# Optimization experiments

Hardware: AMD Instinct MI355X
Metric: run time of the kernel (lower is better)

Reference implementation:

```python
import jax, jax.numpy as jnp
import numpy as np

Z_DIM = 64
K = 2048
N = 32768


def setup_inputs() -> dict:
    key = jax.random.key(0)
    k1, k2 = jax.random.split(key)
    x = jax.random.normal(k1, (N, Z_DIM), dtype=jnp.float32)
    # init.normal_(locs, std=sqrt(z_dim))
    locs = jax.random.normal(k2, (K, Z_DIM), dtype=jnp.float32) * np.sqrt(Z_DIM)
    logits = jnp.zeros((K,), dtype=jnp.float32)  # maxent buffer
    return {"x": x, "locs": locs, "logits": logits}


def reference(x, locs, logits):
    d = x.shape[-1]
    var = jnp.float32(d)  # scale = sqrt(z_dim) -> variance = z_dim
    # squared distances [N, K] via cdist expansion (avoids [N,K,d] intermediate)
    sq = (
        jnp.sum(x * x, axis=-1, keepdims=True)
        + jnp.sum(locs * locs, axis=-1)[None, :]
        - 2.0 * (x @ locs.T)
    )
    # Independent Normal log prob summed over z_dim
    log_norm_const = d * (0.5 * jnp.log(2.0 * jnp.pi) + 0.5 * jnp.log(var))
    comp_log_prob = -0.5 * sq / var - log_norm_const  # [N, K]
    mix_logits = jax.nn.log_softmax(logits)  # Categorical normalizes logits
    wlp = comp_log_prob + mix_logits  # weighted_log_prob, [N, K]
    log_prob = jax.nn.logsumexp(wlp, axis=-1)  # [N]
    modes = jnp.argmax(wlp, axis=-1)  # assign_modes, [N]
    quantized = locs[modes]  # hard_quantize, [N, z_dim]
    return log_prob, quantized
```

## Files before the change

### kernel.cpp

```cpp
#include <hip/hip_runtime.h>
#include <math.h>

#define N_SAMP 32768
#define K_COMP 2048
#define ZD 64
#define LNC 191.896324792608546f
#define LN2F 0.69314718055994531f
#define INV_LN2 1.44269504088896340f
#define S2C 0.02254211001388974f

#define KG 4
#define TILES (K_COMP / 16 / KG)

typedef __attribute__((ext_vector_type(8))) short short8;
typedef __attribute__((ext_vector_type(4))) float v4f;

#if __has_builtin(__builtin_amdgcn_exp2f)
#define EXP2(x) __builtin_amdgcn_exp2f(x)
#else
#define EXP2(x) exp2f(x)
#endif

__device__ inline unsigned short f2bf(float f) {
    unsigned int u = __float_as_uint(f);
    u += 0x7fffu + ((u >> 16) & 1u);
    return (unsigned short)(u >> 16);
}
__device__ inline float bf2f(unsigned short h) {
    return __uint_as_float(((unsigned int)h) << 16);
}

__global__ __launch_bounds__(256) void prep_kernel(
    const float* __restrict__ locs, const float* __restrict__ logits,
    float* __restrict__ ck2, float* __restrict__ lse_out,
    char* __restrict__ lf) {
    if (blockIdx.x < 32) {
        int gid = blockIdx.x * 256 + threadIdx.x;
        int T = gid >> 6;
        int l = gid & 63;
        int n = l & 15, q = l >> 4;
        int k = T * 16 + n;

        const float* src = locs + (size_t)k * ZD + q * 8;
        float4 u0 = *(const float4*)(src);
        float4 u1 = *(const float4*)(src + 4);
        float4 u2 = *(const float4*)(src + 32);
        float4 u3 = *(const float4*)(src + 36);
        float a[8] = {u0.x, u0.y, u0.z, u0.w, u1.x, u1.y, u1.z, u1.w};
        float b[8] = {u2.x, u2.y, u2.z, u2.w, u3.x, u3.y, u3.z, u3.w};

        short8 h0, h1, l0, l1;
        float sq = 0.f;
#pragma unroll
        for (int j = 0; j < 8; ++j) {
            unsigned short ha = f2bf(a[j]);
            h0[j] = (short)ha; l0[j] = (short)f2bf(a[j] - bf2f(ha));
            unsigned short hb = f2bf(b[j]);
            h1[j] = (short)hb; l1[j] = (short)f2bf(b[j] - bf2f(hb));
            sq = fmaf(a[j], a[j], sq);
            sq = fmaf(b[j], b[j], sq);
        }
        char* dst = lf + (size_t)T * 4096 + l * 16;
        *(short8*)(dst)        = h0;
        *(short8*)(dst + 1024) = h1;
        *(short8*)(dst + 2048) = l0;
        *(short8*)(dst + 3072) = l1;

        sq += __shfl_xor(sq, 16);
        sq += __shfl_xor(sq, 32);
        if (q == 0) ck2[k] = (logits[k] - sq * (1.0f / 128.0f)) * INV_LN2;
    } else {
        __shared__ float red[4];
        int tid = threadIdx.x;
        int wv = tid >> 6, ln = tid & 63;
        float lm = -INFINITY;
        for (int i = tid; i < K_COMP; i += 256) lm = fmaxf(lm, logits[i]);
#pragma unroll
        for (int d = 1; d < 64; d <<= 1) lm = fmaxf(lm, __shfl_xor(lm, d));
        if (ln == 0) red[wv] = lm;
        __syncthreads();
        float M = fmaxf(fmaxf(red[0], red[1]), fmaxf(red[2], red[3]));
        float ls = 0.f;
        for (int i = tid; i < K_COMP; i += 256) ls += __expf(logits[i] - M);
#pragma unroll
        for (int d = 1; d < 64; d <<= 1) ls += __shfl_xor(ls, d);
        __syncthreads();
        if (ln == 0) red[wv] = ls;
        __syncthreads();
        if (tid == 0) *lse_out = M + __logf(red[0] + red[1] + red[2] + red[3]);
    }
}

__global__ __launch_bounds__(256, 2) void mix_kernel(
    const float* __restrict__ x, const float* __restrict__ locs,
    const char* __restrict__ lf, const float* __restrict__ ck2,
    const float* __restrict__ lse_ptr, float* __restrict__ out) {

    __shared__ float sm[KG][64];
    __shared__ float ss[KG][64];
    __shared__ int   sa[KG][64];
    __shared__ int   amax_sh[64];

    const int tid  = threadIdx.x;
    const int lane = tid & 63;
    const int kg   = __builtin_amdgcn_readfirstlane(tid >> 6);
    const int n    = lane & 15;
    const int quad = lane >> 4;
    const int sbase = blockIdx.x * 64;

    short8 bh[4][2], bl[4][2];
    float xs[4];
#pragma unroll
    for (int bt = 0; bt < 4; ++bt) {
        const float* xp = x + (size_t)(sbase + bt * 16 + n) * ZD + quad * 8;
        float4 u0 = *(const float4*)(xp);
        float4 u1 = *(const float4*)(xp + 4);
        float4 u2 = *(const float4*)(xp + 32);
        float4 u3 = *(const float4*)(xp + 36);
        float a[8] = {u0.x, u0.y, u0.z, u0.w, u1.x, u1.y, u1.z, u1.w};
        float b[8] = {u2.x, u2.y, u2.z, u2.w, u3.x, u3.y, u3.z, u3.w};
        float p = 0.f;
#pragma unroll
        for (int j = 0; j < 8; ++j) {
            unsigned short h;
            h = f2bf(a[j]); bh[bt][0][j] = (short)h; bl[bt][0][j] = (short)f2bf(a[j] - bf2f(h));
            h = f2bf(b[j]); bh[bt][1][j] = (short)h; bl[bt][1][j] = (short)f2bf(b[j] - bf2f(h));
            p = fmaf(a[j], a[j], p);
            p = fmaf(b[j], b[j], p);
        }
        p += __shfl_xor(p, 16);
        p += __shfl_xor(p, 32);
        xs[bt] = p;
    }

    const char* aw = lf + (size_t)kg * TILES * 4096 + lane * 16;
    const float* ckw = ck2 + kg * TILES * 16 + quad * 4;
    const int kb0 = kg * TILES * 16 + quad * 4;

    short8 fa[2][4];
    float4 fc[2];

#define LOADA(slot, tt) do {                                     \
    const char* _p = aw + (size_t)(tt) * 4096;                   \
    fa[slot][0] = *(const short8*)(_p);                          \
    fa[slot][1] = *(const short8*)(_p + 1024);                   \
    fa[slot][2] = *(const short8*)(_p + 2048);                   \
    fa[slot][3] = *(const short8*)(_p + 3072);                   \
    fc[slot] = *(const float4*)(ckw + (tt) * 16);                \
} while (0)

    float mm[4] = {-1e30f, -1e30f, -1e30f, -1e30f};
    float s0[4] = {0.f, 0.f, 0.f, 0.f};
    float s1[4] = {0.f, 0.f, 0.f, 0.f};
    int   ai[4] = {0, 0, 0, 0};

#define COMPUTE(slot, tt) do {                                                  \
    v4f acc[4];                                                                 \
    _Pragma("unroll")                                                           \
    for (int bt = 0; bt < 4; ++bt) acc[bt] = (v4f){0.f, 0.f, 0.f, 0.f};         \
    _Pragma("unroll")                                                           \
    for (int h = 0; h < 2; ++h) {                                               \
        _Pragma("unroll")                                                       \
        for (int bt = 0; bt < 4; ++bt)                                          \
            acc[bt] = __builtin_amdgcn_mfma_f32_16x16x32_bf16(                  \
                fa[slot][h], bh[bt][h], acc[bt], 0, 0, 0);                      \
    }                                                                           \
    _Pragma("unroll")                                                           \
    for (int h = 0; h < 2; ++h) {                                               \
        _Pragma("unroll")                                                       \
        for (int bt = 0; bt < 4; ++bt)                                          \
            acc[bt] = __builtin_amdgcn_mfma_f32_16x16x32_bf16(                  \
                fa[slot][h], bl[bt][h], acc[bt], 0, 0, 0);                      \
    }                                                                           \
    _Pragma("unroll")                                                           \
    for (int h = 0; h < 2; ++h) {                                               \
        _Pragma("unroll")                                                       \
        for (int bt = 0; bt < 4; ++bt)                                          \
            acc[bt] = __builtin_amdgcn_mfma_f32_16x16x32_bf16(                  \
                fa[slot][2 + h], bh[bt][h], acc[bt], 0, 0, 0);                  \
    }                                                                           \
    const int kb = kb0 + (tt) * 16;                                             \
    float4 cc = fc[slot];                                                       \
    _Pragma("unroll")                                                           \
    for (int bt = 0; bt < 4; ++bt) {                                            \
        float w0 = fmaf(acc[bt].x, S2C, cc.x);                                  \
        float w1 = fmaf(acc[bt].y, S2C, cc.y);                                  \
        float w2 = fmaf(acc[bt].z, S2C, cc.z);                                  \
        float w3 = fmaf(acc[bt].w, S2C, cc.w);                                  \
        s0[bt] += EXP2(w0) + EXP2(w1);                                          \
        s1[bt] += EXP2(w2) + EXP2(w3);                                          \
        float t01 = fmaxf(w0, w1); int i01 = (w1 > w0) ? (kb + 1) : (kb + 0);   \
        float t23 = fmaxf(w2, w3); int i23 = (w3 > w2) ? (kb + 3) : (kb + 2);   \
        float tt2 = fmaxf(t01, t23); int it = (t23 > t01) ? i23 : i01;          \
        ai[bt] = (tt2 > mm[bt]) ? it : ai[bt];                                  \
        mm[bt] = fmaxf(mm[bt], tt2);                                            \
    }                                                                           \
} while (0)

    LOADA(0, 0);
    for (int t = 0; t < TILES; t += 2) {
        int t1 = (t + 1 < TILES) ? (t + 1) : (TILES - 1);
        LOADA(1, t1);
        COMPUTE(0, t);
        int t2 = (t + 2 < TILES) ? (t + 2) : (TILES - 1);
        LOADA(0, t2);
        COMPUTE(1, t + 1);
    }

#pragma unroll
    for (int bt = 0; bt < 4; ++bt) {
        float sum = s0[bt] + s1[bt];
#pragma unroll
        for (int d = 16; d <= 32; d <<= 1) {
            sum += __shfl_xor(sum, d);
            float om = __shfl_xor(mm[bt], d);
            int   oa = __shfl_xor(ai[bt], d);
            ai[bt] = (om > mm[bt] || (om == mm[bt] && oa < ai[bt])) ? oa : ai[bt];
            mm[bt] = fmaxf(mm[bt], om);
        }
        if (quad == 0) {
            sm[kg][bt * 16 + n] = mm[bt];
            ss[kg][bt * 16 + n] = sum;
            sa[kg][bt * 16 + n] = ai[bt];
        }
    }
    __syncthreads();

    if (tid < 64) {
        float M = -1e30f, S = 0.f;
        int A = 0;
#pragma unroll
        for (int k = 0; k < KG; ++k) {
            float mw = sm[k][tid];
            int aw2 = sa[k][tid];
            S += ss[k][tid];
            A = (mw > M || (mw == M && aw2 < A)) ? aw2 : A;
            M = fmaxf(M, mw);
        }
        float myxs = (quad == 0) ? xs[0] : (quad == 1) ? xs[1]
                   : (quad == 2) ? xs[2] : xs[3];
        float bias = -myxs * (1.0f / 128.0f) - LNC;
        out[sbase + tid] = fmaf(__log2f(S), LN2F, bias - lse_ptr[0]);
        amax_sh[tid] = A;
    }
    __syncthreads();

    const float4* lq = (const float4*)locs;
    float4* oq = (float4*)(out + N_SAMP + (size_t)sbase * ZD);
#pragma unroll
    for (int i = tid; i < 64 * (ZD / 4); i += 256) {
        int r = i >> 4, c = i & 15;
        oq[i] = lq[(size_t)amax_sh[r] * (ZD / 4) + c];
    }
#undef LOADA
#undef COMPUTE
}

extern "C" void kernel_launch(void* const* d_in, const int* in_sizes, int n_in,
                              void* d_out, int out_size, void* d_ws, size_t ws_size,
                              hipStream_t stream) {
    const float* x      = (const float*)d_in[0];
    const float* locs   = (const float*)d_in[1];
    const float* logits = (const float*)d_in[2];
    float* out = (float*)d_out;

    float* ck2 = (float*)d_ws;
    float* lse = ck2 + K_COMP;
    char*  lf  = (char*)d_ws + 16384;

    prep_kernel<<<33, 256, 0, stream>>>(locs, logits, ck2, lse, lf);
    mix_kernel<<<N_SAMP / 64, 256, 0, stream>>>(x, locs, lf, ck2, lse, out);
}
```

Before: 95.51 us.

## Share component tiles across waves via LDS with async global-to-LDS double buffering

The work split changes from each wave covering a quarter of the K components for all 64 samples to each wave covering 16 samples across all K components. The precomputed bf16 locs tiles are loaded cooperatively into a double-buffered LDS stage with global_load_lds DMA and read by all four waves, so the block fetches each tile from global memory once instead of each wave fetching its own. The cross-wave shared-memory reduction goes away, but there is now a __syncthreads per stage, and each wave holds one sample tile instead of four, which lowers the MFMA reuse of the A fragments.

Result: slower. 100.4 us (+5.1%).

```diff
diff --git a/kernel.cpp b/kernel.cpp
--- a/kernel.cpp
+++ b/kernel.cpp
@@ -9,8 +9,9 @@
 #define INV_LN2 1.44269504088896340f
 #define S2C 0.02254211001388974f
 
-#define KG 4
-#define TILES (K_COMP / 16 / KG)
+#define TILES_TOT 128
+#define TPS 4
+#define STAGES (TILES_TOT / TPS)
 
 typedef __attribute__((ext_vector_type(8))) short short8;
 typedef __attribute__((ext_vector_type(4))) float v4f;
@@ -20,6 +21,12 @@
 #else
 #define EXP2(x) exp2f(x)
 #endif
+
+typedef const __attribute__((address_space(1))) unsigned int* gas_t;
+typedef __attribute__((address_space(3))) unsigned int* las_t;
+__device__ inline void gload_lds16(const void* g, void* l) {
+    __builtin_amdgcn_global_load_lds((gas_t)g, (las_t)l, 16, 0, 0);
+}
 
 __device__ inline unsigned short f2bf(float f) {
     unsigned int u = __float_as_uint(f);
@@ -96,23 +103,21 @@
     const char* __restrict__ lf, const float* __restrict__ ck2,
     const float* __restrict__ lse_ptr, float* __restrict__ out) {
 
-    __shared__ float sm[KG][64];
-    __shared__ float ss[KG][64];
-    __shared__ int   sa[KG][64];
-    __shared__ int   amax_sh[64];
+    __shared__ char buf[2][TPS * 4096];
+    __shared__ int amax_sh[64];
 
     const int tid  = threadIdx.x;
     const int lane = tid & 63;
-    const int kg   = __builtin_amdgcn_readfirstlane(tid >> 6);
+    const int wv   = __builtin_amdgcn_readfirstlane(tid >> 6);
     const int n    = lane & 15;
     const int quad = lane >> 4;
     const int sbase = blockIdx.x * 64;
-
-    short8 bh[4][2], bl[4][2];
-    float xs[4];
-#pragma unroll
-    for (int bt = 0; bt < 4; ++bt) {
-        const float* xp = x + (size_t)(sbase + bt * 16 + n) * ZD + quad * 8;
+    const int srow  = sbase + wv * 16 + n;
+
+    short8 bh0, bh1, bl0, bl1;
+    float xs;
+    {
+        const float* xp = x + (size_t)srow * ZD + quad * 8;
         float4 u0 = *(const float4*)(xp);
         float4 u1 = *(const float4*)(xp + 4);
         float4 u2 = *(const float4*)(xp + 32);
@@ -123,125 +128,109 @@
 #pragma unroll
         for (int j = 0; j < 8; ++j) {
             unsigned short h;
-            h = f2bf(a[j]); bh[bt][0][j] = (short)h; bl[bt][0][j] = (short)f2bf(a[j] - bf2f(h));
-            h = f2bf(b[j]); bh[bt][1][j] = (short)h; bl[bt][1][j] = (short)f2bf(b[j] - bf2f(h));
+            h = f2bf(a[j]); bh0[j] = (short)h; bl0[j] = (short)f2bf(a[j] - bf2f(h));
+            h = f2bf(b[j]); bh1[j] = (short)h; bl1[j] = (short)f2bf(b[j] - bf2f(h));
             p = fmaf(a[j], a[j], p);
             p = fmaf(b[j], b[j], p);
         }
         p += __shfl_xor(p, 16);
         p += __shfl_xor(p, 32);
-        xs[bt] = p;
-    }
-
-    const char* aw = lf + (size_t)kg * TILES * 4096 + lane * 16;
-    const float* ckw = ck2 + kg * TILES * 16 + quad * 4;
-    const int kb0 = kg * TILES * 16 + quad * 4;
-
-    short8 fa[2][4];
-    float4 fc[2];
-
-#define LOADA(slot, tt) do {                                     \
-    const char* _p = aw + (size_t)(tt) * 4096;                   \
-    fa[slot][0] = *(const short8*)(_p);                          \
-    fa[slot][1] = *(const short8*)(_p + 1024);                   \
-    fa[slot][2] = *(const short8*)(_p + 2048);                   \
-    fa[slot][3] = *(const short8*)(_p + 3072);                   \
-    fc[slot] = *(const float4*)(ckw + (tt) * 16);                \
+        xs = p;
+    }
+
+    const char* gsrc0 = lf + (size_t)wv * 4096 + lane * 16;
+    char* ldst0 = &buf[0][wv * 4096];
+
+#define DMA(S, b) do {                                                   \
+    const char* _g = gsrc0 + (size_t)(S) * (TPS * 4096);                 \
+    char* _l = ldst0 + (b) * (TPS * 4096);                               \
+    gload_lds16(_g, _l);                                                 \
+    gload_lds16(_g + 1024, _l + 1024);                                   \
+    gload_lds16(_g + 2048, _l + 2048);                                   \
+    gload_lds16(_g + 3072, _l + 3072);                                   \
 } while (0)
 
-    float mm[4] = {-1e30f, -1e30f, -1e30f, -1e30f};
-    float s0[4] = {0.f, 0.f, 0.f, 0.f};
-    float s1[4] = {0.f, 0.f, 0.f, 0.f};
-    int   ai[4] = {0, 0, 0, 0};
-
-#define COMPUTE(slot, tt) do {                                                  \
-    v4f acc[4];                                                                 \
-    _Pragma("unroll")                                                           \
-    for (int bt = 0; bt < 4; ++bt) acc[bt] = (v4f){0.f, 0.f, 0.f, 0.f};         \
-    _Pragma("unroll")                                                           \
-    for (int h = 0; h < 2; ++h) {                                               \
-        _Pragma("unroll")                                                       \
-        for (int bt = 0; bt < 4; ++bt)                                          \
-            acc[bt] = __builtin_amdgcn_mfma_f32_16x16x32_bf16(                  \
-                fa[slot][h], bh[bt][h], acc[bt], 0, 0, 0);                      \
-    }                                                                           \
-    _Pragma("unroll")                                                           \
-    for (int h = 0; h < 2; ++h) {                                               \
-        _Pragma("unroll")                                                       \
-        for (int bt = 0; bt < 4; ++bt)                                          \
-            acc[bt] = __builtin_amdgcn_mfma_f32_16x16x32_bf16(                  \
-                fa[slot][h], bl[bt][h], acc[bt], 0, 0, 0);                      \
-    }                                                                           \
-    _Pragma("unroll")                                                           \
-    for (int h = 0; h < 2; ++h) {                                               \
-        _Pragma("unroll")                                                       \
-        for (int bt = 0; bt < 4; ++bt)                                          \
-            acc[bt] = __builtin_amdgcn_mfma_f32_16x16x32_bf16(                  \
-                fa[slot][2 + h], bh[bt][h], acc[bt], 0, 0, 0);                  \
-    }                                                                           \
-    const int kb = kb0 + (tt) * 16;                                             \
-    float4 cc = fc[slot];                                                       \
-    _Pragma("unroll")                                                           \
-    for (int bt = 0; bt < 4; ++bt) {                                            \
-        float w0 = fmaf(acc[bt].x, S2C, cc.x);                                  \
-        float w1 = fmaf(acc[bt].y, S2C, cc.y);                                  \
-        float w2 = fmaf(acc[bt].z, S2C, cc.z);                                  \
-        float w3 = fmaf(acc[bt].w, S2C, cc.w);                                  \
-        s0[bt] += EXP2(w0) + EXP2(w1);                                          \
-        s1[bt] += EXP2(w2) + EXP2(w3);                                          \
-        float t01 = fmaxf(w0, w1); int i01 = (w1 > w0) ? (kb + 1) : (kb + 0);   \
-        float t23 = fmaxf(w2, w3); int i23 = (w3 > w2) ? (kb + 3) : (kb + 2);   \
-        float tt2 = fmaxf(t01, t23); int it = (t23 > t01) ? i23 : i01;          \
-        ai[bt] = (tt2 > mm[bt]) ? it : ai[bt];                                  \
-        mm[bt] = fmaxf(mm[bt], tt2);                                            \
-    }                                                                           \
+    float mm = -1e30f, s0 = 0.f, s1 = 0.f;
+    int ai = 0;
+
+#define EPI(acc, fcv, kb) do {                                                 \
+    float w0 = fmaf((acc).x, S2C, (fcv).x);                                    \
+    float w1 = fmaf((acc).y, S2C, (fcv).y);                                    \
+    float w2 = fmaf((acc).z, S2C, (fcv).z);                                    \
+    float w3 = fmaf((acc).w, S2C, (fcv).w);                                    \
+    s0 += EXP2(w0) + EXP2(w1);                                                 \
+    s1 += EXP2(w2) + EXP2(w3);                                                 \
+    float t01 = fmaxf(w0, w1); int i01 = (w1 > w0) ? ((kb) + 1) : ((kb) + 0);  \
+    float t23 = fmaxf(w2, w3); int i23 = (w3 > w2) ? ((kb) + 3) : ((kb) + 2);  \
+    float tt2 = fmaxf(t01, t23); int it = (t23 > t01) ? i23 : i01;             \
+    ai = (tt2 > mm) ? it : ai;                                                 \
+    mm = fmaxf(mm, tt2);                                                       \
 } while (0)
 
-    LOADA(0, 0);
-    for (int t = 0; t < TILES; t += 2) {
-        int t1 = (t + 1 < TILES) ? (t + 1) : (TILES - 1);
-        LOADA(1, t1);
-        COMPUTE(0, t);
-        int t2 = (t + 2 < TILES) ? (t + 2) : (TILES - 1);
-        LOADA(0, t2);
-        COMPUTE(1, t + 1);
-    }
-
-#pragma unroll
-    for (int bt = 0; bt < 4; ++bt) {
-        float sum = s0[bt] + s1[bt];
-#pragma unroll
-        for (int d = 16; d <= 32; d <<= 1) {
-            sum += __shfl_xor(sum, d);
-            float om = __shfl_xor(mm[bt], d);
-            int   oa = __shfl_xor(ai[bt], d);
-            ai[bt] = (om > mm[bt] || (om == mm[bt] && oa < ai[bt])) ? oa : ai[bt];
-            mm[bt] = fmaxf(mm[bt], om);
+    DMA(0, 0);
+    __syncthreads();
+
+    for (int S = 0; S < STAGES; ++S) {
+        const int b = S & 1;
+        if (S + 1 < STAGES) DMA(S + 1, b ^ 1);
+
+        const float* ckS = ck2 + S * (TPS * 16) + quad * 4;
+        float4 fc0 = *(const float4*)(ckS);
+        float4 fc1 = *(const float4*)(ckS + 16);
+        float4 fc2 = *(const float4*)(ckS + 32);
+        float4 fc3 = *(const float4*)(ckS + 48);
+
+        const char* base = &buf[b][lane * 16];
+        const int kb0 = S * (TPS * 16) + quad * 4;
+
+#pragma unroll
+        for (int j = 0; j < TPS; j += 2) {
+            const char* p0 = base + j * 4096;
+            const char* p1 = base + (j + 1) * 4096;
+            short8 a00 = *(const short8*)(p0);
+            short8 a01 = *(const short8*)(p0 + 1024);
+            short8 a02 = *(const short8*)(p0 + 2048);
+            short8 a03 = *(const short8*)(p0 + 3072);
+            short8 a10 = *(const short8*)(p1);
+            short8 a11 = *(const short8*)(p1 + 1024);
+            short8 a12 = *(const short8*)(p1 + 2048);
+            short8 a13 = *(const short8*)(p1 + 3072);
+
+            v4f ca = {0.f, 0.f, 0.f, 0.f};
+            v4f cb = {0.f, 0.f, 0.f, 0.f};
+            ca = __builtin_amdgcn_mfma_f32_16x16x32_bf16(a00, bh0, ca, 0, 0, 0);
+            cb = __builtin_amdgcn_mfma_f32_16x16x32_bf16(a10, bh0, cb, 0, 0, 0);
+            ca = __builtin_amdgcn_mfma_f32_16x16x32_bf16(a01, bh1, ca, 0, 0, 0);
+            cb = __builtin_amdgcn_mfma_f32_16x16x32_bf16(a11, bh1, cb, 0, 0, 0);
+            ca = __builtin_amdgcn_mfma_f32_16x16x32_bf16(a00, bl0, ca, 0, 0, 0);
+            cb = __builtin_amdgcn_mfma_f32_16x16x32_bf16(a10, bl0, cb, 0, 0, 0);
+            ca = __builtin_amdgcn_mfma_f32_16x16x32_bf16(a01, bl1, ca, 0, 0, 0);
+            cb = __builtin_amdgcn_mfma_f32_16x16x32_bf16(a11, bl1, cb, 0, 0, 0);
+            ca = __builtin_amdgcn_mfma_f32_16x16x32_bf16(a02, bh0, ca, 0, 0, 0);
+            cb = __builtin_amdgcn_mfma_f32_16x16x32_bf16(a12, bh0, cb, 0, 0, 0);
+            ca = __builtin_amdgcn_mfma_f32_16x16x32_bf16(a03, bh1, ca, 0, 0, 0);
+            cb = __builtin_amdgcn_mfma_f32_16x16x32_bf16(a13, bh1, cb, 0, 0, 0);
+
+            if (j == 0) { EPI(ca, fc0, kb0 + 0 * 16); EPI(cb, fc1, kb0 + 1 * 16); }
+            else        { EPI(ca, fc2, kb0 + 2 * 16); EPI(cb, fc3, kb0 + 3 * 16); }
         }
-        if (quad == 0) {
-            sm[kg][bt * 16 + n] = mm[bt];
-            ss[kg][bt * 16 + n] = sum;
-            sa[kg][bt * 16 + n] = ai[bt];
-        }
-    }
-    __syncthreads();
-
-    if (tid < 64) {
-        float M = -1e30f, S = 0.f;
-        int A = 0;
-#pragma unroll
-        for (int k = 0; k < KG; ++k) {
-            float mw = sm[k][tid];
-            int aw2 = sa[k][tid];
-            S += ss[k][tid];
-            A = (mw > M || (mw == M && aw2 < A)) ? aw2 : A;
-            M = fmaxf(M, mw);
-        }
-        float myxs = (quad == 0) ? xs[0] : (quad == 1) ? xs[1]
-                   : (quad == 2) ? xs[2] : xs[3];
-        float bias = -myxs * (1.0f / 128.0f) - LNC;
-        out[sbase + tid] = fmaf(__log2f(S), LN2F, bias - lse_ptr[0]);
-        amax_sh[tid] = A;
+        __syncthreads();
+    }
+
+    float sum = s0 + s1;
+#pragma unroll
+    for (int d = 16; d <= 32; d <<= 1) {
+        sum += __shfl_xor(sum, d);
+        float om = __shfl_xor(mm, d);
+        int   oa = __shfl_xor(ai, d);
+        ai = (om > mm || (om == mm && oa < ai)) ? oa : ai;
+        mm = fmaxf(mm, om);
+    }
+
+    if (quad == 0) {
+        float bias = -xs * (1.0f / 128.0f) - LNC;
+        out[srow] = fmaf(__log2f(sum), LN2F, bias - lse_ptr[0]);
+        amax_sh[wv * 16 + n] = ai;
     }
     __syncthreads();
 
@@ -252,8 +241,8 @@
         int r = i >> 4, c = i & 15;
         oq[i] = lq[(size_t)amax_sh[r] * (ZD / 4) + c];
     }
-#undef LOADA
-#undef COMPUTE
+#undef DMA
+#undef EPI
 }
 
 extern "C" void kernel_launch(void* const* d_in, const int* in_sizes, int n_in,
```
